# Optimization experiments

Hardware: AMD Instinct MI355X
Metric: run time of the kernel (lower is better)

Reference implementation:

```python
import jax, jax.numpy as jnp
import numpy as np
import math

H = 8        # num_heads
DK = 64      # key_dim
DV = 64      # value_dim
FACTOR = 4


def setup_inputs() -> dict:
    key = jax.random.key(0)
    B, T, S, D = 4, 2048, 2048, 512
    Dout = H * DV
    ks = jax.random.split(key, 16)
    sample_k = min(int(FACTOR * math.log(S)), S)  # = 33
    inp = {
        "x_q": jax.random.normal(ks[0], (B, T, D), jnp.float32),
        "x_k": jax.random.normal(ks[1], (B, S, D), jnp.float32),
        "x_v": jax.random.normal(ks[2], (B, S, D), jnp.float32),
        "Wq": jax.random.normal(ks[3], (D, H * DK), jnp.float32) * 0.02,
        "bq": jnp.zeros((H * DK,), jnp.float32),
        "Wk": jax.random.normal(ks[4], (D, H * DK), jnp.float32) * 0.02,
        "bk": jnp.zeros((H * DK,), jnp.float32),
        "Wv": jax.random.normal(ks[5], (D, H * DV), jnp.float32) * 0.02,
        "bv": jnp.zeros((H * DV,), jnp.float32),
        "Wo": jax.random.normal(ks[6], (H * DV, Dout), jnp.float32) * 0.02,
        "bo": jnp.zeros((Dout,), jnp.float32),
        "index_sample": jax.random.randint(ks[7], (T, sample_k), 0, S, jnp.int32),
    }
    return inp


def reference(x_q, x_k, x_v, Wq, bq, Wk, bk, Wv, bv, Wo, bo, index_sample):
    B, T, D = x_q.shape
    S = x_k.shape[1]
    u = min(int(FACTOR * math.log(T)), T)  # n_top queries kept

    q = (x_q @ Wq + bq).reshape(B, T, H, DK)
    k = (x_k @ Wk + bk).reshape(B, S, H, DK)
    v = (x_v @ Wv + bv).reshape(B, S, H, DV)

    # --- _prob_QK: sampled QK to score queries ---
    ks = k[:, index_sample]                                  # [B,T,J,H,dk]
    qk_s = jnp.einsum('bthd,btjhd->bthj', q, ks)             # [B,T,H,J]
    M = qk_s.max(-1) - qk_s.mean(-1)                         # [B,T,H]
    _, top = jax.lax.top_k(jnp.transpose(M, (0, 2, 1)), u)   # [B,H,u]

    b_idx = jnp.arange(B)[:, None, None]
    h_idx = jnp.arange(H)[None, :, None]
    q_red = q[b_idx, top, h_idx]                             # [B,H,u,dk]
    qk = jnp.einsum('bhud,bshd->bhus', q_red, k)             # [B,H,u,S]

    # --- s0: default (no mask) context = mean of values over S ---
    ctx = jnp.broadcast_to(v.mean(axis=1, keepdims=True), (B, T, H, DV))
    ctx = jnp.transpose(ctx, (0, 2, 1, 3))                   # [B,H,T,dv]

    # --- s1: scaled softmax over full keys for top queries ---
    scores = jax.nn.softmax(qk * (1.0 / math.sqrt(DK)), axis=-1)
    attn = jnp.einsum('bhus,bshd->bhud', scores, v)          # [B,H,u,dv]

    # --- scatter top-query results into context / scores ---
    ctx = ctx.at[b_idx, h_idx, top].set(attn)                # [B,H,T,dv]
    final_scores = jnp.full((B, H, T, S), 1.0 / S, dtype=scores.dtype)
    final_scores = final_scores.at[b_idx, h_idx, top].set(scores)

    out = jnp.transpose(ctx, (0, 2, 1, 3)).reshape(B, T, H * DV)
    out = out @ Wo + bo                                      # [B,T,output_dim]
    return out, final_scores
```

## Files before the change

kernel.cpp:

```cpp
#include <hip/hip_runtime.h>

typedef __attribute__((ext_vector_type(8))) short short8;
typedef __attribute__((ext_vector_type(4))) float f32x4;

constexpr int Bn  = 4;
constexpr int Tn  = 2048;
constexpr int Sn  = 2048;
constexpr int Dn  = 512;
constexpr int Hn  = 8;
constexpr int DKn = 64;
constexpr int DVn = 64;
constexpr int HDn = 512;
constexpr int SKn = 30;
constexpr int Un  = 30;
constexpr int Gu  = 6;
constexpr int NGroups = Un / Gu;
constexpr int NAttnG  = Bn * Hn * NGroups;
constexpr int NOutF   = (Bn * Tn) / 8;
constexpr int NGemm  = 768;
constexpr float kScale = 0.125f;

constexpr int NWsplit = 192;
constexpr int NVPart  = 64;
constexpr int NSampled = Bn * Tn;

constexpr int NFillG = 9216;
constexpr int NFillS = 4608;
constexpr int NFillT = 2560;
constexpr int FillRowsG = 0;
constexpr int FillRowsS = NFillG * 4;
constexpr int FillRowsT = (NFillG + NFillS) * 4;

__device__ __forceinline__ ushort bf16_rne(float x) {
  unsigned u = __float_as_uint(x);
  return (ushort)((u + 0x7fffu + ((u >> 16) & 1u)) >> 16);
}
__device__ __forceinline__ float bf16f(ushort h) {
  return __uint_as_float(((unsigned)h) << 16);
}
__device__ __forceinline__ void nt_store4(f32x4* p, f32x4 v) {
  __builtin_nontemporal_store(v, p);
}
__device__ __forceinline__ void fill_rows4_256(float* fscores, size_t r0, int tid) {
  const float c = 1.0f / Sn;
  const f32x4 c4v = {c, c, c, c};
  f32x4* fs4 = (f32x4*)fscores + r0 * (Sn / 4);
#pragma unroll
  for (int i = 0; i < 8; ++i) nt_store4(fs4 + i * 256 + tid, c4v);
}

#define MFMA(accv, av, bv) \
  asm volatile("v_mfma_f32_16x16x32_bf16 %0, %1, %2, %0" : "+v"(accv) : "v"(av), "v"(bv))

__global__ __launch_bounds__(256) void prep_split_kernel(
    const float* __restrict__ Wq, const float* __restrict__ Wk, const float* __restrict__ Wv,
    ushort* __restrict__ WtH, ushort* __restrict__ WtL) {
  const int tid = threadIdx.x;
  const int bid = blockIdx.x;

  const int z = bid / 64, t = bid % 64;
  const int k0 = (t >> 3) * 64, n0 = (t & 7) * 64;
  const float* W = (z == 0) ? Wq : (z == 1) ? Wk : Wv;
  __shared__ float tile[64][65];
  const int r = tid >> 2, c0 = (tid & 3) * 16;
#pragma unroll
  for (int i = 0; i < 16; i += 4) {
    const float4 vv = *(const float4*)(W + (size_t)(k0 + r) * HDn + n0 + c0 + i);
    tile[r][c0 + i] = vv.x; tile[r][c0 + i + 1] = vv.y;
    tile[r][c0 + i + 2] = vv.z; tile[r][c0 + i + 3] = vv.w;
  }
  __syncthreads();
  unsigned hp[8], lp[8];
#pragma unroll
  for (int i = 0; i < 16; i += 2) {
    const float x0 = tile[c0 + i][r];
    const float x1 = tile[c0 + i + 1][r];
    const ushort h0 = bf16_rne(x0), h1 = bf16_rne(x1);
    const ushort l0 = bf16_rne(x0 - bf16f(h0)), l1 = bf16_rne(x1 - bf16f(h1));
    hp[i >> 1] = (unsigned)h0 | ((unsigned)h1 << 16);
    lp[i >> 1] = (unsigned)l0 | ((unsigned)l1 << 16);
  }
  const size_t off = (size_t)(z * 512 + n0 + r) * 512 + k0 + c0;
  *(uint4*)(WtH + off)     = make_uint4(hp[0], hp[1], hp[2], hp[3]);
  *(uint4*)(WtH + off + 8) = make_uint4(hp[4], hp[5], hp[6], hp[7]);
  *(uint4*)(WtL + off)     = make_uint4(lp[0], lp[1], lp[2], lp[3]);
  *(uint4*)(WtL + off + 8) = make_uint4(lp[4], lp[5], lp[6], lp[7]);
}

__global__ __launch_bounds__(256, 2) void gemm_fill_kernel(
    const float* __restrict__ xq, const float* __restrict__ xk, const float* __restrict__ xv,
    const ushort* __restrict__ WtH, const ushort* __restrict__ WtL,
    const float* __restrict__ bq, const float* __restrict__ bk, const float* __restrict__ bv,
    float* __restrict__ qo, float* __restrict__ ko, float* __restrict__ vo,
    float* __restrict__ fscores) {
  const int bid = blockIdx.x;
  const int tid = threadIdx.x;

  if (bid >= NGemm) {
    fill_rows4_256(fscores, (size_t)FillRowsG + (size_t)(bid - NGemm) * 4, tid);
    return;
  }

  __shared__ ushort AsH[64][32];
  __shared__ ushort AsL[64][32];
  __shared__ ushort BsH[256][32];
  __shared__ ushort BsL[256][32];

  const int z = bid >> 8;
  const int rem = bid & 255;
  const int bm = (rem >> 1) * 64;
  const int bn = (rem & 1) * 256;
  const float* X = (z == 0) ? xq : (z == 1) ? xk : xv;
  const float* bias = (z == 0) ? bq : (z == 1) ? bk : bv;
  float* Y = (z == 0) ? qo : (z == 1) ? ko : vo;

  const int lane = tid & 63;
  const int wave = tid >> 6;
  const int fr = lane & 15;
  const int gk = lane >> 4;

  const int ar = tid >> 2, ag = tid & 3;
  const float* xrow = X + (size_t)(bm + ar) * Dn + ag * 8;
  const int brow0 = tid >> 2, bg = tid & 3;
  const ushort* wh = WtH + (size_t)(z * 512 + bn + brow0) * 512 + bg * 8;
  const ushort* wl = WtL + (size_t)(z * 512 + bn + brow0) * 512 + bg * 8;

  f32x4 acc[4][4];
#pragma unroll
  for (int m = 0; m < 4; ++m)
#pragma unroll
    for (int n = 0; n < 4; ++n)
#pragma unroll
      for (int j = 0; j < 4; ++j) acc[m][n][j] = 0.f;

  float4 af0, af1;
  uint4 sbH[4], sbL[4];
#define STG_LOAD(k0_) do { \
    af0 = *(const float4*)(xrow + (k0_)); \
    af1 = *(const float4*)(xrow + (k0_) + 4); \
    sbH[0] = *(const uint4*)(wh + (k0_));          sbL[0] = *(const uint4*)(wl + (k0_)); \
    sbH[1] = *(const uint4*)(wh + (k0_) + 32768);  sbL[1] = *(const uint4*)(wl + (k0_) + 32768); \
    sbH[2] = *(const uint4*)(wh + (k0_) + 65536);  sbL[2] = *(const uint4*)(wl + (k0_) + 65536); \
    sbH[3] = *(const uint4*)(wh + (k0_) + 98304);  sbL[3] = *(const uint4*)(wl + (k0_) + 98304); \
  } while (0)

  const int agq = (ag ^ ((ar >> 1) & 3)) * 8;
  const int bgx = bg ^ ((brow0 >> 1) & 3);
  const int gq = (gk ^ ((fr >> 1) & 3)) * 8;

  STG_LOAD(0);
  for (int k0 = 0; k0 < Dn; k0 += 32) {
    __syncthreads();
    {
      float xf[8] = {af0.x, af0.y, af0.z, af0.w, af1.x, af1.y, af1.z, af1.w};
      unsigned hp[4], lp[4];
#pragma unroll
      for (int i = 0; i < 8; i += 2) {
        const ushort h0 = bf16_rne(xf[i]), h1 = bf16_rne(xf[i + 1]);
        const ushort l0 = bf16_rne(xf[i] - bf16f(h0)), l1 = bf16_rne(xf[i + 1] - bf16f(h1));
        hp[i >> 1] = (unsigned)h0 | ((unsigned)h1 << 16);
        lp[i >> 1] = (unsigned)l0 | ((unsigned)l1 << 16);
      }
      *(uint4*)&AsH[ar][agq] = make_uint4(hp[0], hp[1], hp[2], hp[3]);
      *(uint4*)&AsL[ar][agq] = make_uint4(lp[0], lp[1], lp[2], lp[3]);
#pragma unroll
      for (int p = 0; p < 4; ++p) {
        const int n = brow0 + p * 64;
        *(uint4*)&BsH[n][bgx * 8] = sbH[p];
        *(uint4*)&BsL[n][bgx * 8] = sbL[p];
      }
    }
    __syncthreads();
    if (k0 + 32 < Dn) STG_LOAD(k0 + 32);

    short8 aH[4], aL[4], bH[4], bL[4];
#pragma unroll
    for (int m = 0; m < 4; ++m) {
      aH[m] = *(const short8*)&AsH[m * 16 + fr][gq];
      aL[m] = *(const short8*)&AsL[m * 16 + fr][gq];
    }
#pragma unroll
    for (int n = 0; n < 4; ++n) {
      bH[n] = *(const short8*)&BsH[wave * 64 + n * 16 + fr][gq];
      bL[n] = *(const short8*)&BsL[wave * 64 + n * 16 + fr][gq];
    }
#pragma unroll
    for (int m = 0; m < 4; ++m)
#pragma unroll
      for (int n = 0; n < 4; ++n) {
        MFMA(acc[m][n], aH[m], bH[n]);
        MFMA(acc[m][n], aH[m], bL[n]);
        MFMA(acc[m][n], aL[m], bH[n]);
      }
  }
  asm volatile("s_nop 7\n\ts_nop 7");

  float bsv[4];
#pragma unroll
  for (int n = 0; n < 4; ++n) bsv[n] = bias[bn + wave * 64 + n * 16 + fr];
#pragma unroll
  for (int m = 0; m < 4; ++m) {
#pragma unroll
    for (int n = 0; n < 4; ++n) {
      const int col = bn + wave * 64 + n * 16 + fr;
#pragma unroll
      for (int j = 0; j < 4; ++j) {
        Y[(size_t)(bm + m * 16 + gk * 4 + j) * HDn + col] = acc[m][n][j] + bsv[n];
      }
    }
  }
#undef STG_LOAD
}

__global__ __launch_bounds__(64) void sampled_m_kernel(
    const float* __restrict__ q, const float* __restrict__ k,
    const int* __restrict__ idxs, float* __restrict__ Mt,
    const float* __restrict__ v, float* __restrict__ vpart,
    float* __restrict__ fscores) {
  const int bid = blockIdx.x;
  const int lane = threadIdx.x;

  if (bid >= NVPart + NSampled) {
    const size_t r0 = (size_t)FillRowsS + (size_t)(bid - NVPart - NSampled) * 4;
    const float c = 1.0f / Sn;
    const f32x4 c4v = {c, c, c, c};
    f32x4* p = (f32x4*)fscores + r0 * (Sn / 4);
#pragma unroll
    for (int i = 0; i < 32; ++i) nt_store4(p + i * 64 + lane, c4v);
    return;
  }

  if (bid < NVPart) {
    const int pb = bid;
    const int b = pb >> 4, part = pb & 15;
    const float4* v4 = (const float4*)(v + (size_t)b * Sn * HDn);
    float4 a0 = make_float4(0.f, 0.f, 0.f, 0.f);
    float4 a1 = make_float4(0.f, 0.f, 0.f, 0.f);
    const int s0 = part * 128;
    for (int s = s0; s < s0 + 128; ++s) {
      const float4 x0 = v4[(size_t)s * 128 + lane * 2];
      const float4 x1 = v4[(size_t)s * 128 + lane * 2 + 1];
      a0.x += x0.x; a0.y += x0.y; a0.z += x0.z; a0.w += x0.w;
      a1.x += x1.x; a1.y += x1.y; a1.z += x1.z; a1.w += x1.w;
    }
    float4* vp4 = (float4*)vpart + (size_t)pb * 128;
    vp4[lane * 2] = a0; vp4[lane * 2 + 1] = a1;
    return;
  }

  const int inner = bid - NVPart;
  const int b = inner >> 11, t = inner & (Tn - 1);

  const int sg = lane >> 3;
  const int d8 = lane & 7;
  __shared__ int sidx[32];
  if (lane < SKn) sidx[lane] = idxs[t * SKn + lane];
  if (lane >= SKn && lane < 32) sidx[lane] = 0;
  __syncthreads();
  const float* qrow = q + ((size_t)(b * Tn + t)) * HDn;
  const float* kb = k + (size_t)b * Sn * HDn;
  for (int h = 0; h < Hn; ++h) {
    const float4 qv0 = *(const float4*)(qrow + h * DKn + d8 * 8);
    const float4 qv1 = *(const float4*)(qrow + h * DKn + d8 * 8 + 4);
    float mx = -1e30f, sum = 0.f;
#pragma unroll
    for (int jb = 0; jb < 32; jb += 8) {
      const int j = jb + sg;
      const int srow = sidx[j];
      const float* kr = kb + (size_t)srow * HDn + h * DKn + d8 * 8;
      const float4 kv0 = *(const float4*)kr;
      const float4 kv1 = *(const float4*)(kr + 4);
      float p = kv0.x * qv0.x + kv0.y * qv0.y + kv0.z * qv0.z + kv0.w * qv0.w
              + kv1.x * qv1.x + kv1.y * qv1.y + kv1.z * qv1.z + kv1.w * qv1.w;
      p += __shfl_xor(p, 1);
      p += __shfl_xor(p, 2);
      p += __shfl_xor(p, 4);
      if (j < SKn) { mx = fmaxf(mx, p); sum += p; }
    }
    mx = fmaxf(mx, __shfl_xor(mx, 8));
    mx = fmaxf(mx, __shfl_xor(mx, 16));
    mx = fmaxf(mx, __shfl_xor(mx, 32));
    sum += __shfl_xor(sum, 8);
    sum += __shfl_xor(sum, 16);
    sum += __shfl_xor(sum, 32);
    if (lane == 0) Mt[((size_t)(b * Hn + h)) * Tn + t] = mx - sum * (1.0f / SKn);
  }
}

__global__ __launch_bounds__(256) void topk_vmean_base_kernel(
    const float* __restrict__ Mt, const float* __restrict__ vpart,
    const float* __restrict__ Wo, const float* __restrict__ bo,
    int* __restrict__ top, float* __restrict__ vmean, float* __restrict__ basep,
    float* __restrict__ fscores) {
  const int tid = threadIdx.x;
  const int lane = tid & 63, w = tid >> 6;

  if (blockIdx.x >= 36) {
    fill_rows4_256(fscores, (size_t)FillRowsT + (size_t)(blockIdx.x - 36) * 4, tid);
    return;
  }

  __shared__ float vals[Tn];
  __shared__ float wv[4];
  __shared__ int wi[4];
  __shared__ float4 part[256];
  __shared__ float vm[HDn];

  if (blockIdx.x < 32) {
    const int bh = blockIdx.x;
    for (int i = tid; i < Tn; i += 256) vals[i] = Mt[(size_t)bh * Tn + i];
    __syncthreads();
    for (int u = 0; u < Un; ++u) {
      float bv = -1e30f; int bi = 0x7fffffff;
      for (int i = tid; i < Tn; i += 256) {
        const float x = vals[i];
        if (x > bv) { bv = x; bi = i; }
      }
#pragma unroll
      for (int o = 1; o < 64; o <<= 1) {
        const float ov = __shfl_xor(bv, o);
        const int oi = __shfl_xor(bi, o);
        if (ov > bv || (ov == bv && oi < bi)) { bv = ov; bi = oi; }
      }
      if (lane == 0) { wv[w] = bv; wi[w] = bi; }
      __syncthreads();
      bv = wv[0]; bi = wi[0];
#pragma unroll
      for (int j = 1; j < 4; ++j) {
        if (wv[j] > bv || (wv[j] == bv && wi[j] < bi)) { bv = wv[j]; bi = wi[j]; }
      }
      if (tid == 0) { top[bh * Un + u] = bi; vals[bi] = -1e30f; }
      __syncthreads();
    }
  } else {
    const int b = blockIdx.x - 32;
    const int c4 = tid & 127, half = tid >> 7;
    float4 acc = make_float4(0.f, 0.f, 0.f, 0.f);
    for (int p = half * 8; p < half * 8 + 8; ++p) {
      const float4 x = ((const float4*)vpart)[(size_t)(b * 16 + p) * 128 + c4];
      acc.x += x.x; acc.y += x.y; acc.z += x.z; acc.w += x.w;
    }
    part[tid] = acc;
    __syncthreads();
    if (half == 0) {
      float4 a = part[c4], bpp = part[128 + c4];
      const float sc = 1.0f / Sn;
      float4 r = make_float4((a.x + bpp.x) * sc, (a.y + bpp.y) * sc,
                             (a.z + bpp.z) * sc, (a.w + bpp.w) * sc);
      *(float4*)(vm + c4 * 4) = r;
      *(float4*)(vmean + b * HDn + c4 * 4) = r;
    }
    __syncthreads();
    const float4* Wo4 = (const float4*)Wo;
    float4 acc2 = make_float4(0.f, 0.f, 0.f, 0.f);
    for (int c = half * 256; c < half * 256 + 256; ++c) {
      const float vmc = vm[c];
      const float4 wrow = Wo4[(size_t)c * 128 + c4];
      acc2.x += vmc * wrow.x; acc2.y += vmc * wrow.y;
      acc2.z += vmc * wrow.z; acc2.w += vmc * wrow.w;
    }
    __syncthreads();
    part[tid] = acc2;
    __syncthreads();
    if (half == 0) {
      float4 a = part[c4], bpp = part[128 + c4];
      const float4 bb = ((const float4*)bo)[c4];
      float4 r = make_float4(a.x + bpp.x + bb.x, a.y + bpp.y + bb.y,
                             a.z + bpp.z + bb.z, a.w + bpp.w + bb.w);
      ((float4*)basep)[b * 128 + c4] = r;
    }
  }
}

__global__ __launch_bounds__(256) void attn_out_kernel(
    const float* __restrict__ q, const float* __restrict__ k,
    const float* __restrict__ v, const float* __restrict__ vmean,
    const int* __restrict__ top, const float* __restrict__ Wo,
    const float* __restrict__ basep,
    float* __restrict__ out, float* __restrict__ fscores) {
  const int tid = threadIdx.x;
  const int bid = blockIdx.x;

  if (bid >= NAttnG) {
    const int fid = bid - NAttnG;
    const int r0 = fid * 8;
    const int b = r0 >> 11;
    const int t0 = r0 & (Tn - 1);
    __shared__ int sflag8[8];
    if (tid < 8) sflag8[tid] = 0;
    __syncthreads();
    if (tid < Hn * Un) {
      const int d = top[b * Hn * Un + tid] - t0;
      if (d >= 0 && d < 8) sflag8[d] = 1;
    }
    __syncthreads();
    const int col4 = tid & 127, rh = tid >> 7;
    const float4 bv4 = ((const float4*)basep)[b * 128 + col4];
    const f32x4 bvx = {bv4.x, bv4.y, bv4.z, bv4.w};
#pragma unroll
    for (int rp = 0; rp < 4; ++rp) {
      const int rr = rp * 2 + rh;
      float4* orow4 = (float4*)(out + (size_t)(r0 + rr) * HDn) + col4;
      if (sflag8[rr]) {
        float* p = (float*)orow4;
        atomicAdd(p + 0, bv4.x); atomicAdd(p + 1, bv4.y);
        atomicAdd(p + 2, bv4.z); atomicAdd(p + 3, bv4.w);
      } else {
        nt_store4((f32x4*)orow4, bvx);
      }
    }
    return;
  }

  const int xs = bid & 7;
  const int b = xs & 3;
  const int combo = (bid >> 3) + (xs >> 2) * 20;
  const int h = combo / 5;
  const int grp = combo % 5;
  const int bh = b * Hn + h;
  const int u0 = grp * Gu;
  const int lane = tid & 63, w = tid >> 6;

  __shared__ float qs[Gu][DKn];
  __shared__ float sc[Gu][2052];
  __shared__ float red[8];
  __shared__ int tsel[Gu];
  __shared__ float4 partv[4][Gu][16];

  if (tid < Gu) tsel[tid] = top[bh * Un + u0 + tid];
  __syncthreads();
  for (int i = tid; i < Gu * DKn; i += 256) {
    const int g = i >> 6, d = i & 63;
    qs[g][d] = q[((size_t)(b * Tn + tsel[g])) * HDn + h * DKn + d];
  }
  __syncthreads();

  const float4* k4 = (const float4*)k;
  for (int s = tid; s < Sn; s += 256) {
    const float4* krow = k4 + ((size_t)(b * Sn + s)) * 128 + h * 16;
    float acc[Gu];
#pragma unroll
    for (int g = 0; g < Gu; ++g) acc[g] = 0.f;
#pragma unroll
    for (int d4i = 0; d4i < 16; ++d4i) {
      const float4 kv = krow[d4i];
#pragma unroll
      for (int g = 0; g < Gu; ++g) {
        const float4 qv = *(const float4*)&qs[g][d4i * 4];
        acc[g] += kv.x * qv.x + kv.y * qv.y + kv.z * qv.z + kv.w * qv.w;
      }
    }
#pragma unroll
    for (int g = 0; g < Gu; ++g) sc[g][s] = acc[g] * kScale;
  }
  __syncthreads();

  float invs[Gu];
#pragma unroll
  for (int g = 0; g < Gu; ++g) {
    float lm = -1e30f;
    for (int i = tid; i < Sn; i += 256) lm = fmaxf(lm, sc[g][i]);
#pragma unroll
    for (int o = 1; o < 64; o <<= 1) lm = fmaxf(lm, __shfl_xor(lm, o));
    if (lane == 0) red[w] = lm;
    __syncthreads();
    const float mx = fmaxf(fmaxf(red[0], red[1]), fmaxf(red[2], red[3]));
    float ls = 0.f;
    for (int i = tid; i < Sn; i += 256) {
      const float e = __expf(sc[g][i] - mx);
      sc[g][i] = e;
      ls += e;
    }
#pragma unroll
    for (int o = 1; o < 64; o <<= 1) ls += __shfl_xor(ls, o);
    if (lane == 0) red[4 + w] = ls;
    __syncthreads();
    invs[g] = 1.0f / (red[4] + red[5] + red[6] + red[7]);
    __syncthreads();
  }
#pragma unroll
  for (int g = 0; g < Gu; ++g) {
    const float inv = invs[g];
    float4* scg4 = (float4*)sc[g];
    f32x4* fsrow4 = (f32x4*)(fscores + ((size_t)bh * Tn + tsel[g]) * Sn);
#pragma unroll
    for (int it = 0; it < 2; ++it) {
      const int i = it * 256 + tid;
      float4 p = scg4[i];
      p.x *= inv; p.y *= inv; p.z *= inv; p.w *= inv;
      scg4[i] = p;
      const f32x4 px = {p.x, p.y, p.z, p.w};
      nt_store4(fsrow4 + i, px);
    }
  }
  __syncthreads();

  const int d4 = lane & 15;
  const int sg = (w << 2) + (lane >> 4);
  const float4* v4 = (const float4*)v;
  float4 pacc[Gu];
#pragma unroll
  for (int g = 0; g < Gu; ++g) pacc[g] = make_float4(0.f, 0.f, 0.f, 0.f);
  for (int s = sg; s < Sn; s += 16) {
    const float4 vv = v4[((size_t)(b * Sn + s)) * 128 + h * 16 + d4];
#pragma unroll
    for (int g = 0; g < Gu; ++g) {
      const float p = sc[g][s];
      pacc[g].x += p * vv.x; pacc[g].y += p * vv.y;
      pacc[g].z += p * vv.z; pacc[g].w += p * vv.w;
    }
  }
#pragma unroll
  for (int g = 0; g < Gu; ++g) {
#pragma unroll
    for (int o = 16; o < 64; o <<= 1) {
      pacc[g].x += __shfl_xor(pacc[g].x, o);
      pacc[g].y += __shfl_xor(pacc[g].y, o);
      pacc[g].z += __shfl_xor(pacc[g].z, o);
      pacc[g].w += __shfl_xor(pacc[g].w, o);
    }
    if (lane < 16) partv[w][g][lane] = pacc[g];
  }
  __syncthreads();
  if (tid < Gu * 16) {
    const int g = tid >> 4, dd = tid & 15;
    float4 r = partv[0][g][dd];
    const float4 r1 = partv[1][g][dd], r2 = partv[2][g][dd], r3 = partv[3][g][dd];
    r.x += r1.x + r2.x + r3.x; r.y += r1.y + r2.y + r3.y;
    r.z += r1.z + r2.z + r3.z; r.w += r1.w + r2.w + r3.w;
    const float4 vm4 = ((const float4*)vmean)[bh * 16 + dd];
    r.x -= vm4.x; r.y -= vm4.y; r.z -= vm4.z; r.w -= vm4.w;
    *(float4*)&qs[g][dd * 4] = r;
  }
  __syncthreads();

  const int col4 = tid & 127, gg = tid >> 7;
  const float4* Wo4 = (const float4*)Wo;
#pragma unroll
  for (int gp = 0; gp < Gu / 2; ++gp) {
    const int g = gp * 2 + gg;
    float4 a = make_float4(0.f, 0.f, 0.f, 0.f);
#pragma unroll
    for (int d = 0; d < DKn; ++d) {
      const float dv = qs[g][d];
      const float4 wrow = Wo4[(size_t)(h * DKn + d) * 128 + col4];
      a.x += dv * wrow.x; a.y += dv * wrow.y;
      a.z += dv * wrow.z; a.w += dv * wrow.w;
    }
    float* orow = out + ((size_t)(b * Tn + tsel[g])) * HDn + col4 * 4;
    atomicAdd(orow + 0, a.x); atomicAdd(orow + 1, a.y);
    atomicAdd(orow + 2, a.z); atomicAdd(orow + 3, a.w);
  }
}

extern "C" void kernel_launch(void* const* d_in, const int* in_sizes, int n_in,
                              void* d_out, int out_size, void* d_ws, size_t ws_size,
                              hipStream_t stream) {
  const float* x_q = (const float*)d_in[0];
  const float* x_k = (const float*)d_in[1];
  const float* x_v = (const float*)d_in[2];
  const float* Wq = (const float*)d_in[3];
  const float* bq = (const float*)d_in[4];
  const float* Wk = (const float*)d_in[5];
  const float* bk = (const float*)d_in[6];
  const float* Wv = (const float*)d_in[7];
  const float* bv = (const float*)d_in[8];
  const float* Wo = (const float*)d_in[9];
  const float* bo = (const float*)d_in[10];
  const int* idx = (const int*)d_in[11];

  float* out = (float*)d_out;
  float* fscores = out + (size_t)Bn * Tn * HDn;

  float* ws = (float*)d_ws;
  float* q = ws;
  float* kp = ws + (size_t)4194304;
  float* vp = ws + (size_t)8388608;
  float* Mt = ws + (size_t)12582912;
  float* vmean = ws + (size_t)12648448;
  float* basep = ws + (size_t)12650496;
  int* top = (int*)(ws + (size_t)12652544);
  float* vpart = ws + (size_t)12656640;

  char* scr = (char*)(fscores + (size_t)49152 * Sn);
  ushort* WtH = (ushort*)scr;
  ushort* WtL = WtH + (size_t)3 * 512 * 512;

  prep_split_kernel<<<NWsplit, 256, 0, stream>>>(Wq, Wk, Wv, WtH, WtL);

  gemm_fill_kernel<<<NGemm + NFillG, 256, 0, stream>>>(
      x_q, x_k, x_v, WtH, WtL, bq, bk, bv, q, kp, vp, fscores);

  sampled_m_kernel<<<NVPart + NSampled + NFillS, 64, 0, stream>>>(
      q, kp, idx, Mt, vp, vpart, fscores);

  topk_vmean_base_kernel<<<36 + NFillT, 256, 0, stream>>>(
      Mt, vpart, Wo, bo, top, vmean, basep, fscores);

  attn_out_kernel<<<NAttnG + NOutF, 256, 0, stream>>>(
      q, kp, vp, vmean, top, Wo, basep, out, fscores);
}
```

Before: 894.3 us.

## Load projection weight tiles directly into LDS via global_load_lds and rebalance fill

The bf16 hi/lo weight tiles in the QKV projection GEMM now go straight from global memory into shared memory through the global_load_lds builtin. This replaces the old path of loading into registers and then storing to LDS, which should cut register pressure and VALU/LDS store work. The register prefetch of the next weight tile is dropped, so the B loads are now issued and waited on inside the same iteration, with only the A activations still prefetched. The split of the constant-score fill work is also moved from the GEMM kernel to the tail kernel.

```diff
diff --git a/kernel.cpp b/kernel.cpp
--- a/kernel.cpp
+++ b/kernel.cpp
@@ -24,9 +24,9 @@
 constexpr int NVPart  = 64;
 constexpr int NSampled = Bn * Tn;
 
-constexpr int NFillG = 9216;
+constexpr int NFillG = 7168;
 constexpr int NFillS = 4608;
-constexpr int NFillT = 2560;
+constexpr int NFillT = 4608;
 constexpr int FillRowsG = 0;
 constexpr int FillRowsS = NFillG * 4;
 constexpr int FillRowsT = (NFillG + NFillS) * 4;
@@ -47,6 +47,10 @@
   f32x4* fs4 = (f32x4*)fscores + r0 * (Sn / 4);
 #pragma unroll
   for (int i = 0; i < 8; ++i) nt_store4(fs4 + i * 256 + tid, c4v);
+}
+__device__ __forceinline__ void gload_lds16(const void* g, void* lds) {
+  __builtin_amdgcn_global_load_lds((const __attribute__((address_space(1))) void*)g,
+                                   (__attribute__((address_space(3))) void*)lds, 16, 0, 0);
 }
 
 #define MFMA(accv, av, bv) \
@@ -121,9 +125,15 @@
 
   const int ar = tid >> 2, ag = tid & 3;
   const float* xrow = X + (size_t)(bm + ar) * Dn + ag * 8;
-  const int brow0 = tid >> 2, bg = tid & 3;
-  const ushort* wh = WtH + (size_t)(z * 512 + bn + brow0) * 512 + bg * 8;
-  const ushort* wl = WtL + (size_t)(z * 512 + bn + brow0) * 512 + bg * 8;
+  const int agq = (ag ^ ((ar >> 1) & 3)) * 8;
+
+  const int gsrc = (lane & 3) ^ ((lane >> 3) & 3);
+  const ushort* bgH = WtH + (size_t)(z * 512 + bn + wave * 64 + (lane >> 2)) * 512 + gsrc * 8;
+  const ushort* bgL = WtL + (size_t)(z * 512 + bn + wave * 64 + (lane >> 2)) * 512 + gsrc * 8;
+  ushort* ldsH0 = &BsH[wave * 64][0];
+  ushort* ldsL0 = &BsL[wave * 64][0];
+
+  const int gq = (gk ^ ((fr >> 1) & 3)) * 8;
 
   f32x4 acc[4][4];
 #pragma unroll
@@ -133,24 +143,16 @@
 #pragma unroll
       for (int j = 0; j < 4; ++j) acc[m][n][j] = 0.f;
 
-  float4 af0, af1;
-  uint4 sbH[4], sbL[4];
-#define STG_LOAD(k0_) do { \
-    af0 = *(const float4*)(xrow + (k0_)); \
-    af1 = *(const float4*)(xrow + (k0_) + 4); \
-    sbH[0] = *(const uint4*)(wh + (k0_));          sbL[0] = *(const uint4*)(wl + (k0_)); \
-    sbH[1] = *(const uint4*)(wh + (k0_) + 32768);  sbL[1] = *(const uint4*)(wl + (k0_) + 32768); \
-    sbH[2] = *(const uint4*)(wh + (k0_) + 65536);  sbL[2] = *(const uint4*)(wl + (k0_) + 65536); \
-    sbH[3] = *(const uint4*)(wh + (k0_) + 98304);  sbL[3] = *(const uint4*)(wl + (k0_) + 98304); \
-  } while (0)
-
-  const int agq = (ag ^ ((ar >> 1) & 3)) * 8;
-  const int bgx = bg ^ ((brow0 >> 1) & 3);
-  const int gq = (gk ^ ((fr >> 1) & 3)) * 8;
-
-  STG_LOAD(0);
+  float4 af0 = *(const float4*)(xrow + 0);
+  float4 af1 = *(const float4*)(xrow + 4);
+
   for (int k0 = 0; k0 < Dn; k0 += 32) {
     __syncthreads();
+#pragma unroll
+    for (int c = 0; c < 4; ++c) {
+      gload_lds16(bgH + k0 + c * 8192, ldsH0 + c * 512);
+      gload_lds16(bgL + k0 + c * 8192, ldsL0 + c * 512);
+    }
     {
       float xf[8] = {af0.x, af0.y, af0.z, af0.w, af1.x, af1.y, af1.z, af1.w};
       unsigned hp[4], lp[4];
@@ -163,15 +165,12 @@
       }
       *(uint4*)&AsH[ar][agq] = make_uint4(hp[0], hp[1], hp[2], hp[3]);
       *(uint4*)&AsL[ar][agq] = make_uint4(lp[0], lp[1], lp[2], lp[3]);
-#pragma unroll
-      for (int p = 0; p < 4; ++p) {
-        const int n = brow0 + p * 64;
-        *(uint4*)&BsH[n][bgx * 8] = sbH[p];
-        *(uint4*)&BsL[n][bgx * 8] = sbL[p];
-      }
-    }
-    __syncthreads();
-    if (k0 + 32 < Dn) STG_LOAD(k0 + 32);
+    }
+    if (k0 + 32 < Dn) {
+      af0 = *(const float4*)(xrow + k0 + 32);
+      af1 = *(const float4*)(xrow + k0 + 36);
+    }
+    __syncthreads();
 
     short8 aH[4], aL[4], bH[4], bL[4];
 #pragma unroll
@@ -209,7 +208,6 @@
       }
     }
   }
-#undef STG_LOAD
 }
 
 __global__ __launch_bounds__(64) void sampled_m_kernel(
```

Result: faster. 765.5 us (-14.4%).
